# Optimization experiments

Measured on AMD Instinct MI355X. Metric: run time of the kernel, lower is better.

The kernel has to match this reference:

```python
import jax, jax.numpy as jnp
import numpy as np

N_NODES = 50000


def _gcn_conv(x, W, b, src, dst, n):
    # GCNConv (PyG semantics): x' = D^-1/2 (A + I) D^-1/2 (x W) + b
    h = x @ W  # [N, out]
    loop = jnp.arange(n, dtype=src.dtype)
    s = jnp.concatenate([src, loop])  # self-loops appended
    d = jnp.concatenate([dst, loop])
    deg = jax.ops.segment_sum(jnp.ones_like(d, dtype=h.dtype), d, num_segments=n)
    dinv = jnp.where(deg > 0, jax.lax.rsqrt(deg), 0.0)
    norm = dinv[s] * dinv[d]  # [E+N]
    msgs = norm[:, None] * h[s]  # gather: [E+N, out]
    out = jax.ops.segment_sum(msgs, d, num_segments=n)  # scatter-add
    return out + b


def setup_inputs() -> dict:
    key = jax.random.key(0)
    ks = jax.random.split(key, 6)
    n, din, dh, dout, e = N_NODES, 64, 64, 16, 1600000
    x = jax.random.normal(ks[0], (n, din), dtype=jnp.float32)
    edge_index = jax.random.randint(ks[1], (2, e), 0, n, dtype=jnp.int64)
    W1 = jax.random.normal(ks[2], (din, dh), dtype=jnp.float32) / np.sqrt(din)
    b1 = jnp.zeros((dh,), dtype=jnp.float32)
    W2 = jax.random.normal(ks[3], (dh, dout), dtype=jnp.float32) / np.sqrt(dh)
    b2 = jnp.zeros((dout,), dtype=jnp.float32)
    return {"x": x, "edge_index": edge_index, "W1": W1, "b1": b1, "W2": W2, "b2": b2}


def reference(x, edge_index, W1, b1, W2, b2):
    n = x.shape[0]
    src, dst = edge_index[0], edge_index[1]
    h = _gcn_conv(x, W1, b1, src, dst, n)
    h = jax.nn.relu(h)
    h = _gcn_conv(h, W2, b2, src, dst, n)
    return jax.nn.log_softmax(h, axis=1)
```

## Files before the change

### kernel.cpp

```cpp
#include <hip/hip_runtime.h>
#include <hip/hip_bf16.h>
#include <math.h>

#define BSHIFT 6
#define BNODES 64
#define MAXB 1024
#define SORTCAP 4096

__device__ __forceinline__ bool detect_f64(const void* edges, long long nn) {
    const long long* e64 = (const long long*)edges;
    bool ok = true;
#pragma unroll
    for (int i = 0; i < 8; ++i) {
        long long v = e64[i];
        ok = ok && (v >= 0 && v < nn);
    }
    return ok;
}

__device__ __forceinline__ float bf16lo(unsigned int u) {
    return __uint_as_float(u << 16);
}
__device__ __forceinline__ float bf16hi(unsigned int u) {
    return __uint_as_float(u & 0xFFFF0000u);
}
__device__ __forceinline__ float bf16dec(unsigned short u) {
    return __uint_as_float(((unsigned int)u) << 16);
}
__device__ __forceinline__ unsigned short bf16enc(float f) {
    __hip_bfloat16 h = __float2bfloat16(f);
    return *reinterpret_cast<unsigned short*>(&h);
}

__global__ __launch_bounds__(256) void k_hist_gemm1(const void* edges, long long nn,
                                                    long long E, long long epb,
                                                    int nbuckets, int nblk, int* partial,
                                                    const float* __restrict__ x,
                                                    const float* __restrict__ W1,
                                                    unsigned short* __restrict__ h1b) {
    __shared__ __align__(16) char smem[20480];
    int t = threadIdx.x;
    if (blockIdx.x < (unsigned int)nblk) {
        int* cnt = (int*)smem;
        int i = blockIdx.x;
        for (int b = t; b < nbuckets; b += 256) cnt[b] = 0;
        __syncthreads();
        bool f64 = detect_f64(edges, nn);
        long long e0 = (long long)i * epb;
        long long e1 = e0 + epb; if (e1 > E) e1 = E;
        for (long long e = e0 + t; e < e1; e += 256) {
            int d = f64 ? (int)((const long long*)edges)[E + e] : ((const int*)edges)[E + e];
            atomicAdd(&cnt[d >> BSHIFT], 1);
        }
        __syncthreads();
        for (int b = t; b < nbuckets; b += 256) partial[b * nblk + i] = cnt[b];
    } else {
        float (*Ws)[64] = (float(*)[64])smem;
        float (*xs)[64] = (float(*)[64])(smem + 64 * 64 * 4);
        for (int i = t; i < 64 * 64; i += 256) Ws[i >> 6][i & 63] = W1[i];
        long long row0 = (long long)(blockIdx.x - nblk) * 16;
        ((float4*)xs)[t] = ((const float4*)(x + row0 * 64))[t];
        __syncthreads();
        int r = t >> 4, c0 = (t & 15) * 4;
        float4 acc = {0.f, 0.f, 0.f, 0.f};
#pragma unroll
        for (int k = 0; k < 64; ++k) {
            float xv = xs[r][k];
            float4 wv = *((const float4*)&Ws[k][c0]);
            acc.x += xv * wv.x; acc.y += xv * wv.y;
            acc.z += xv * wv.z; acc.w += xv * wv.w;
        }
        ushort4 pk;
        pk.x = bf16enc(acc.x);
        pk.y = bf16enc(acc.y);
        pk.z = bf16enc(acc.z);
        pk.w = bf16enc(acc.w);
        *((ushort4*)(h1b + (row0 + r) * 64 + c0)) = pk;
    }
}

__global__ __launch_bounds__(256) void k_scanB(int* partial, int nblk, int* totals) {
    __shared__ int tmp[256];
    int b = blockIdx.x, t = threadIdx.x;
    int v = (t < nblk) ? partial[b * nblk + t] : 0;
    tmp[t] = v;
    __syncthreads();
    for (int off = 1; off < 256; off <<= 1) {
        int a = (t >= off) ? tmp[t - off] : 0;
        __syncthreads();
        tmp[t] += a;
        __syncthreads();
    }
    if (t < nblk) partial[b * nblk + t] = tmp[t] - v;
    if (t == 255) totals[b] = tmp[255];
}

__global__ __launch_bounds__(1024) void k_scan(const int* __restrict__ totals, int nbuckets,
                                               int* base) {
    __shared__ int tmp[MAXB];
    int t = threadIdx.x;
    int v = (t < nbuckets) ? totals[t] : 0;
    tmp[t] = v;
    __syncthreads();
    for (int off = 1; off < MAXB; off <<= 1) {
        int a = (t >= off) ? tmp[t - off] : 0;
        __syncthreads();
        tmp[t] += a;
        __syncthreads();
    }
    if (t < nbuckets) base[t] = tmp[t] - v;
}

__global__ __launch_bounds__(512) void k_place(const void* edges, long long nn,
                                               long long E, long long epb,
                                               int nbuckets, int nblk,
                                               const int* __restrict__ base,
                                               const int* __restrict__ partial,
                                               unsigned int* keys) {
    __shared__ int cur[MAXB];
    int t = threadIdx.x;
    int i = blockIdx.x;
    for (int b = t; b < nbuckets; b += 512) cur[b] = base[b] + partial[b * nblk + i];
    __syncthreads();
    bool f64 = detect_f64(edges, nn);
    long long e0 = (long long)i * epb;
    long long e1 = e0 + epb; if (e1 > E) e1 = E;
    for (long long e = e0 + t; e < e1; e += 512) {
        int s, d;
        if (f64) {
            const long long* ee = (const long long*)edges;
            s = (int)ee[e]; d = (int)ee[E + e];
        } else {
            const int* ee = (const int*)edges;
            s = ee[e]; d = ee[E + e];
        }
        int pos = atomicAdd(&cur[d >> BSHIFT], 1);
        keys[pos] = (unsigned int)s | ((unsigned int)(d & (BNODES - 1)) << 17);
    }
}

__global__ __launch_bounds__(256) void k_sortdeg(unsigned int* keys,
                                                 const int* __restrict__ base,
                                                 const int* __restrict__ totals,
                                                 int* rowstart, int* counts,
                                                 float* dinv, int n,
                                                 unsigned int* scratch) {
    __shared__ unsigned int kbuf[SORTCAP];
    __shared__ int hist[BNODES];
    __shared__ int cur[BNODES];
    int t = threadIdx.x;
    int bk = blockIdx.x;
    int st = base[bk], c = totals[bk];
    if (t < BNODES) hist[t] = 0;
    __syncthreads();
    bool fits = (c <= SORTCAP);
    if (fits) {
        for (int i = t; i < c; i += 256) {
            unsigned int k = keys[st + i];
            kbuf[i] = k;
            atomicAdd(&hist[k >> 17], 1);
        }
    } else {
        for (int i = t; i < c; i += 256) {
            unsigned int k = keys[st + i];
            scratch[st + i] = k;
            atomicAdd(&hist[k >> 17], 1);
        }
    }
    __syncthreads();
    if (t < 64) {
        int v = hist[t];
        int incl = v;
        for (int o = 1; o < 64; o <<= 1) {
            int other = __shfl_up(incl, o, 64);
            if (t >= o) incl += other;
        }
        int ex = incl - v;
        cur[t] = ex;
        int node = bk * BNODES + t;
        if (node < n) {
            rowstart[node] = st + ex;
            counts[node] = v;
            dinv[node] = rsqrtf((float)v + 1.0f);
        }
    }
    __syncthreads();
    if (fits) {
        for (int i = t; i < c; i += 256) {
            unsigned int k = kbuf[i];
            int pos = atomicAdd(&cur[k >> 17], 1);
            keys[st + pos] = k & 0x1FFFFu;
        }
    } else {
        for (int i = t; i < c; i += 256) {
            unsigned int k = scratch[st + i];
            int pos = atomicAdd(&cur[k >> 17], 1);
            keys[st + pos] = k & 0x1FFFFu;
        }
    }
}

__global__ __launch_bounds__(256) void k_agg64(const int* __restrict__ rowstart,
                                               const int* __restrict__ counts,
                                               const unsigned int* __restrict__ srcs,
                                               const uint2* __restrict__ hb4,
                                               const float* __restrict__ dinv,
                                               const float* __restrict__ b,
                                               const float* __restrict__ W2,
                                               unsigned short* __restrict__ h2b, int n) {
    __shared__ float W2s[64 * 17];
    int t = threadIdx.x;
    for (int i = t; i < 64 * 16; i += 256) W2s[(i >> 4) * 17 + (i & 15)] = W2[i];
    __syncthreads();

    int d = (blockIdx.x * 256 + t) >> 6;
    if (d >= n) return;
    int lane = t & 63;
    unsigned int q = lane >> 4;
    unsigned int fl = lane & 15;
    float di = dinv[d];
    float a0 = 0.f, a1 = 0.f, a2 = 0.f, a3 = 0.f;
    if (q == 0) {
        uint2 u = hb4[(unsigned int)d * 16u + fl];
        a0 = di * bf16lo(u.x); a1 = di * bf16hi(u.x);
        a2 = di * bf16lo(u.y); a3 = di * bf16hi(u.y);
    }
    int start = rowstart[d];
    int cnt = counts[d];
    int k = 0;
    for (; k + 16 <= cnt; k += 16) {
        unsigned int s0 = srcs[start + k + q];
        unsigned int s1 = srcs[start + k + 4 + q];
        unsigned int s2 = srcs[start + k + 8 + q];
        unsigned int s3 = srcs[start + k + 12 + q];
        float dv0 = dinv[s0];
        float dv1 = dinv[s1];
        float dv2 = dinv[s2];
        float dv3 = dinv[s3];
        uint2 u0 = hb4[s0 * 16u + fl];
        uint2 u1 = hb4[s1 * 16u + fl];
        uint2 u2 = hb4[s2 * 16u + fl];
        uint2 u3 = hb4[s3 * 16u + fl];
        a0 = fmaf(dv0, bf16lo(u0.x), a0); a1 = fmaf(dv0, bf16hi(u0.x), a1);
        a2 = fmaf(dv0, bf16lo(u0.y), a2); a3 = fmaf(dv0, bf16hi(u0.y), a3);
        a0 = fmaf(dv1, bf16lo(u1.x), a0); a1 = fmaf(dv1, bf16hi(u1.x), a1);
        a2 = fmaf(dv1, bf16lo(u1.y), a2); a3 = fmaf(dv1, bf16hi(u1.y), a3);
        a0 = fmaf(dv2, bf16lo(u2.x), a0); a1 = fmaf(dv2, bf16hi(u2.x), a1);
        a2 = fmaf(dv2, bf16lo(u2.y), a2); a3 = fmaf(dv2, bf16hi(u2.y), a3);
        a0 = fmaf(dv3, bf16lo(u3.x), a0); a1 = fmaf(dv3, bf16hi(u3.x), a1);
        a2 = fmaf(dv3, bf16lo(u3.y), a2); a3 = fmaf(dv3, bf16hi(u3.y), a3);
    }
    for (; k + 8 <= cnt; k += 8) {
        unsigned int s0 = srcs[start + k + q];
        unsigned int s1 = srcs[start + k + 4 + q];
        float dv0 = dinv[s0];
        float dv1 = dinv[s1];
        uint2 u0 = hb4[s0 * 16u + fl];
        uint2 u1 = hb4[s1 * 16u + fl];
        a0 = fmaf(dv0, bf16lo(u0.x), a0); a1 = fmaf(dv0, bf16hi(u0.x), a1);
        a2 = fmaf(dv0, bf16lo(u0.y), a2); a3 = fmaf(dv0, bf16hi(u0.y), a3);
        a0 = fmaf(dv1, bf16lo(u1.x), a0); a1 = fmaf(dv1, bf16hi(u1.x), a1);
        a2 = fmaf(dv1, bf16lo(u1.y), a2); a3 = fmaf(dv1, bf16hi(u1.y), a3);
    }
    for (; k < cnt; k += 4) {
        int idx = k + (int)q;
        if (idx < cnt) {
            unsigned int s0 = srcs[start + idx];
            float dv0 = dinv[s0];
            uint2 u0 = hb4[s0 * 16u + fl];
            a0 = fmaf(dv0, bf16lo(u0.x), a0); a1 = fmaf(dv0, bf16hi(u0.x), a1);
            a2 = fmaf(dv0, bf16lo(u0.y), a2); a3 = fmaf(dv0, bf16hi(u0.y), a3);
        }
    }
    a0 += __shfl_xor(a0, 16); a0 += __shfl_xor(a0, 32);
    a1 += __shfl_xor(a1, 16); a1 += __shfl_xor(a1, 32);
    a2 += __shfl_xor(a2, 16); a2 += __shfl_xor(a2, 32);
    a3 += __shfl_xor(a3, 16); a3 += __shfl_xor(a3, 32);
    float4 bb = ((const float4*)b)[fl];
    float o0 = fmaxf(di * a0 + bb.x, 0.f);
    float o1 = fmaxf(di * a1 + bb.y, 0.f);
    float o2 = fmaxf(di * a2 + bb.z, 0.f);
    float o3 = fmaxf(di * a3 + bb.w, 0.f);

    int c = lane & 15;
    float acc = 0.f;
#pragma unroll
    for (int j = 0; j < 16; ++j) {
        int kk = (int)q * 16 + j;
        int srcl = (int)q * 20 + (j >> 2);
        float fv;
        if ((j & 3) == 0)      fv = __shfl(o0, srcl);
        else if ((j & 3) == 1) fv = __shfl(o1, srcl);
        else if ((j & 3) == 2) fv = __shfl(o2, srcl);
        else                   fv = __shfl(o3, srcl);
        acc += fv * W2s[kk * 17 + c];
    }
    acc += __shfl_xor(acc, 16);
    acc += __shfl_xor(acc, 32);
    if (lane < 16) h2b[(unsigned int)d * 16u + c] = bf16enc(di * acc);
}

__global__ __launch_bounds__(256) void k_agg16(const int* __restrict__ rowstart,
                                               const int* __restrict__ counts,
                                               const unsigned int* __restrict__ srcs,
                                               const unsigned short* __restrict__ hb,
                                               const float* __restrict__ dinv,
                                               const float* __restrict__ b,
                                               float* __restrict__ out, int n) {
    int g = (blockIdx.x * 256 + threadIdx.x) >> 4;
    if (g >= n) return;
    unsigned int f = threadIdx.x & 15;
    float acc = bf16dec(hb[(unsigned int)g * 16u + f]);
    int start = rowstart[g];
    int cnt = counts[g];
    int k = 0;
    for (; k + 8 <= cnt; k += 8) {
        unsigned int s0 = srcs[start + k];
        unsigned int s1 = srcs[start + k + 1];
        unsigned int s2 = srcs[start + k + 2];
        unsigned int s3 = srcs[start + k + 3];
        unsigned int s4 = srcs[start + k + 4];
        unsigned int s5 = srcs[start + k + 5];
        unsigned int s6 = srcs[start + k + 6];
        unsigned int s7 = srcs[start + k + 7];
        unsigned short u0 = hb[s0 * 16u + f];
        unsigned short u1 = hb[s1 * 16u + f];
        unsigned short u2 = hb[s2 * 16u + f];
        unsigned short u3 = hb[s3 * 16u + f];
        unsigned short u4 = hb[s4 * 16u + f];
        unsigned short u5 = hb[s5 * 16u + f];
        unsigned short u6 = hb[s6 * 16u + f];
        unsigned short u7 = hb[s7 * 16u + f];
        acc += bf16dec(u0); acc += bf16dec(u1); acc += bf16dec(u2); acc += bf16dec(u3);
        acc += bf16dec(u4); acc += bf16dec(u5); acc += bf16dec(u6); acc += bf16dec(u7);
    }
    for (; k < cnt; ++k) acc += bf16dec(hb[srcs[start + k] * 16u + f]);
    float v = dinv[g] * acc + b[f];
    float m = v;
#pragma unroll
    for (int o = 8; o >= 1; o >>= 1) m = fmaxf(m, __shfl_xor(m, o, 16));
    float ex = __expf(v - m);
#pragma unroll
    for (int o = 8; o >= 1; o >>= 1) ex += __shfl_xor(ex, o, 16);
    out[(unsigned int)g * 16u + f] = (v - m) - __logf(ex);
}

extern "C" void kernel_launch(void* const* d_in, const int* in_sizes, int n_in,
                              void* d_out, int out_size, void* d_ws, size_t ws_size,
                              hipStream_t stream) {
    const float* x  = (const float*)d_in[0];
    const void*  ei = d_in[1];
    const float* W1 = (const float*)d_in[2];
    const float* b1 = (const float*)d_in[3];
    const float* W2 = (const float*)d_in[4];
    const float* b2 = (const float*)d_in[5];

    long long dh  = in_sizes[3];
    long long din = in_sizes[2] / dh;
    long long n   = in_sizes[0] / din;
    long long E   = (long long)in_sizes[1] / 2;
    int nbuckets  = (int)((n + BNODES - 1) >> BSHIFT);

    long long epb = 8192;
    while ((E + epb - 1) / epb > 256) epb <<= 1;
    int nblk = (int)((E + epb - 1) / epb);
    int ngemm = (int)(n / 16);

    char* ws = (char*)d_ws;
    auto alloc = [&](size_t bytes) { void* p = ws; ws += (bytes + 255) & ~255ULL; return p; };
    int*   totals   = (int*)alloc(nbuckets * 4);
    int*   base     = (int*)alloc(nbuckets * 4);
    int*   rowstart = (int*)alloc(n * 4);
    int*   counts   = (int*)alloc(n * 4);
    float* dinv     = (float*)alloc(n * 4);
    int*   partial  = (int*)alloc((size_t)nbuckets * nblk * 4);
    unsigned int* keys = (unsigned int*)alloc(E * 4);
    unsigned short* h1b  = (unsigned short*)alloc(n * 64 * 2);
    unsigned short* h2b  = (unsigned short*)alloc(n * 16 * 2);
    unsigned int* sort_scratch = (unsigned int*)alloc(E * 4);

    float* out = (float*)d_out;

    k_hist_gemm1<<<nblk + ngemm, 256, 0, stream>>>(ei, n, E, epb, nbuckets, nblk,
                                                   partial, x, W1, h1b);
    k_scanB<<<nbuckets, 256, 0, stream>>>(partial, nblk, totals);
    k_scan<<<1, 1024, 0, stream>>>(totals, nbuckets, base);
    k_place<<<nblk, 512, 0, stream>>>(ei, n, E, epb, nbuckets, nblk, base, partial, keys);
    k_sortdeg<<<nbuckets, 256, 0, stream>>>(keys, base, totals, rowstart, counts,
                                            dinv, (int)n, sort_scratch);

    k_agg64<<<(int)((n * 64 + 255) / 256), 256, 0, stream>>>(
        rowstart, counts, keys, (const uint2*)h1b, dinv, b1, W2, h2b, (int)n);

    k_agg16<<<(int)((n * 16 + 255) / 256), 256, 0, stream>>>(
        rowstart, counts, keys, h2b, dinv, b2, out, (int)n);
}
```

Before: 110.6 us.

## Fold the bucket-total scan into k_place and k_sortdeg, dropping the k_scan launch

Removes the single-block k_scan kernel. Each k_place block now recomputes the exclusive scan of bucket totals itself, with 256 threads covering four buckets each. Each k_sortdeg block finds its start offset by summing the totals of all earlier buckets with a shared-memory tree reduction. This saves one kernel launch and its serialization point. In exchange, the scan work is repeated in every block, and k_place drops from 512 to 256 threads per block.

Result: slower. 113.0 us (+2.2%).

```diff
diff --git a/kernel.cpp b/kernel.cpp
--- a/kernel.cpp
+++ b/kernel.cpp
@@ -95,37 +95,40 @@
     if (t == 255) totals[b] = tmp[255];
 }
 
-__global__ __launch_bounds__(1024) void k_scan(const int* __restrict__ totals, int nbuckets,
-                                               int* base) {
-    __shared__ int tmp[MAXB];
-    int t = threadIdx.x;
-    int v = (t < nbuckets) ? totals[t] : 0;
-    tmp[t] = v;
-    __syncthreads();
-    for (int off = 1; off < MAXB; off <<= 1) {
-        int a = (t >= off) ? tmp[t - off] : 0;
-        __syncthreads();
-        tmp[t] += a;
-        __syncthreads();
-    }
-    if (t < nbuckets) base[t] = tmp[t] - v;
-}
-
-__global__ __launch_bounds__(512) void k_place(const void* edges, long long nn,
+__global__ __launch_bounds__(256) void k_place(const void* edges, long long nn,
                                                long long E, long long epb,
                                                int nbuckets, int nblk,
-                                               const int* __restrict__ base,
+                                               const int* __restrict__ totals,
                                                const int* __restrict__ partial,
                                                unsigned int* keys) {
     __shared__ int cur[MAXB];
+    __shared__ int tmp[256];
     int t = threadIdx.x;
     int i = blockIdx.x;
-    for (int b = t; b < nbuckets; b += 512) cur[b] = base[b] + partial[b * nblk + i];
+    int i0 = t * 4;
+    int x0 = (i0 + 0 < nbuckets) ? totals[i0 + 0] : 0;
+    int x1 = (i0 + 1 < nbuckets) ? totals[i0 + 1] : 0;
+    int x2 = (i0 + 2 < nbuckets) ? totals[i0 + 2] : 0;
+    int x3 = (i0 + 3 < nbuckets) ? totals[i0 + 3] : 0;
+    int s4 = x0 + x1 + x2 + x3;
+    tmp[t] = s4;
+    __syncthreads();
+    for (int off = 1; off < 256; off <<= 1) {
+        int a = (t >= off) ? tmp[t - off] : 0;
+        __syncthreads();
+        tmp[t] += a;
+        __syncthreads();
+    }
+    int ex = tmp[t] - s4;
+    if (i0 + 0 < nbuckets) cur[i0 + 0] = ex + partial[(i0 + 0) * nblk + i];
+    if (i0 + 1 < nbuckets) cur[i0 + 1] = ex + x0 + partial[(i0 + 1) * nblk + i];
+    if (i0 + 2 < nbuckets) cur[i0 + 2] = ex + x0 + x1 + partial[(i0 + 2) * nblk + i];
+    if (i0 + 3 < nbuckets) cur[i0 + 3] = ex + x0 + x1 + x2 + partial[(i0 + 3) * nblk + i];
     __syncthreads();
     bool f64 = detect_f64(edges, nn);
     long long e0 = (long long)i * epb;
     long long e1 = e0 + epb; if (e1 > E) e1 = E;
-    for (long long e = e0 + t; e < e1; e += 512) {
+    for (long long e = e0 + t; e < e1; e += 256) {
         int s, d;
         if (f64) {
             const long long* ee = (const long long*)edges;
@@ -140,7 +143,6 @@
 }
 
 __global__ __launch_bounds__(256) void k_sortdeg(unsigned int* keys,
-                                                 const int* __restrict__ base,
                                                  const int* __restrict__ totals,
                                                  int* rowstart, int* counts,
                                                  float* dinv, int n,
@@ -148,11 +150,20 @@
     __shared__ unsigned int kbuf[SORTCAP];
     __shared__ int hist[BNODES];
     __shared__ int cur[BNODES];
+    __shared__ int rtmp[256];
     int t = threadIdx.x;
     int bk = blockIdx.x;
-    int st = base[bk], c = totals[bk];
+    int psum = 0;
+    for (int b = t; b < bk; b += 256) psum += totals[b];
+    rtmp[t] = psum;
     if (t < BNODES) hist[t] = 0;
     __syncthreads();
+    for (int off = 128; off > 0; off >>= 1) {
+        if (t < off) rtmp[t] += rtmp[t + off];
+        __syncthreads();
+    }
+    int st = rtmp[0];
+    int c = totals[bk];
     bool fits = (c <= SORTCAP);
     if (fits) {
         for (int i = t; i < c; i += 256) {
@@ -369,7 +380,6 @@
     char* ws = (char*)d_ws;
     auto alloc = [&](size_t bytes) { void* p = ws; ws += (bytes + 255) & ~255ULL; return p; };
     int*   totals   = (int*)alloc(nbuckets * 4);
-    int*   base     = (int*)alloc(nbuckets * 4);
     int*   rowstart = (int*)alloc(n * 4);
     int*   counts   = (int*)alloc(n * 4);
     float* dinv     = (float*)alloc(n * 4);
@@ -384,9 +394,8 @@
     k_hist_gemm1<<<nblk + ngemm, 256, 0, stream>>>(ei, n, E, epb, nbuckets, nblk,
                                                    partial, x, W1, h1b);
     k_scanB<<<nbuckets, 256, 0, stream>>>(partial, nblk, totals);
-    k_scan<<<1, 1024, 0, stream>>>(totals, nbuckets, base);
-    k_place<<<nblk, 512, 0, stream>>>(ei, n, E, epb, nbuckets, nblk, base, partial, keys);
-    k_sortdeg<<<nbuckets, 256, 0, stream>>>(keys, base, totals, rowstart, counts,
+    k_place<<<nblk, 256, 0, stream>>>(ei, n, E, epb, nbuckets, nblk, totals, partial, keys);
+    k_sortdeg<<<nbuckets, 256, 0, stream>>>(keys, totals, rowstart, counts,
                                             dinv, (int)n, sort_scratch);
 
     k_agg64<<<(int)((n * 64 + 255) / 256), 256, 0, stream>>>(
```

## Split layer-1 aggregation into two feature-half passes for cache locality

Applied to the files above, without the earlier changes.

Stores the layer-1 bf16 features as two separate 32-column tables and runs the gather-aggregate twice, once per half. Each table is 3.2MB instead of 6.4MB, so the random neighbour gathers are meant to hit in L2/LLC more often. The first pass writes its post-ReLU half to a temporary buffer, and the second pass reads it back to do the W2 projection. In exchange, the edge list, dinv lookups and kernel launches are doubled, and each gather now fetches 4 bytes per lane instead of 8.

Result: slower. 132.6 us (+19.9%).

```diff
diff --git a/kernel.cpp b/kernel.cpp
--- a/kernel.cpp
+++ b/kernel.cpp
@@ -37,7 +37,8 @@
                                                     int nbuckets, int nblk, int* partial,
                                                     const float* __restrict__ x,
                                                     const float* __restrict__ W1,
-                                                    unsigned short* __restrict__ h1b) {
+                                                    unsigned short* __restrict__ h1lo,
+                                                    unsigned short* __restrict__ h1hi) {
     __shared__ __align__(16) char smem[20480];
     int t = threadIdx.x;
     if (blockIdx.x < (unsigned int)nblk) {
@@ -75,7 +76,9 @@
         pk.y = bf16enc(acc.y);
         pk.z = bf16enc(acc.z);
         pk.w = bf16enc(acc.w);
-        *((ushort4*)(h1b + (row0 + r) * 64 + c0)) = pk;
+        unsigned short* dst = (c0 < 32) ? (h1lo + (row0 + r) * 32 + c0)
+                                        : (h1hi + (row0 + r) * 32 + (c0 - 32));
+        *((ushort4*)dst) = pk;
     }
 }
 
@@ -200,30 +203,23 @@
     }
 }
 
-__global__ __launch_bounds__(256) void k_agg64(const int* __restrict__ rowstart,
-                                               const int* __restrict__ counts,
-                                               const unsigned int* __restrict__ srcs,
-                                               const uint2* __restrict__ hb4,
-                                               const float* __restrict__ dinv,
-                                               const float* __restrict__ b,
-                                               const float* __restrict__ W2,
-                                               unsigned short* __restrict__ h2b, int n) {
-    __shared__ float W2s[64 * 17];
-    int t = threadIdx.x;
-    for (int i = t; i < 64 * 16; i += 256) W2s[(i >> 4) * 17 + (i & 15)] = W2[i];
-    __syncthreads();
-
-    int d = (blockIdx.x * 256 + t) >> 6;
+__global__ __launch_bounds__(256) void k_agg64A(const int* __restrict__ rowstart,
+                                                const int* __restrict__ counts,
+                                                const unsigned int* __restrict__ srcs,
+                                                const unsigned int* __restrict__ tbl,
+                                                const float* __restrict__ dinv,
+                                                const float* __restrict__ b,
+                                                unsigned int* __restrict__ outA, int n) {
+    int d = (blockIdx.x * 256 + threadIdx.x) >> 6;
     if (d >= n) return;
-    int lane = t & 63;
+    int lane = threadIdx.x & 63;
     unsigned int q = lane >> 4;
     unsigned int fl = lane & 15;
     float di = dinv[d];
-    float a0 = 0.f, a1 = 0.f, a2 = 0.f, a3 = 0.f;
+    float a0 = 0.f, a1 = 0.f;
     if (q == 0) {
-        uint2 u = hb4[(unsigned int)d * 16u + fl];
-        a0 = di * bf16lo(u.x); a1 = di * bf16hi(u.x);
-        a2 = di * bf16lo(u.y); a3 = di * bf16hi(u.y);
+        unsigned int u = tbl[(unsigned int)d * 16u + fl];
+        a0 = di * bf16lo(u); a1 = di * bf16hi(u);
     }
     int start = rowstart[d];
     int cnt = counts[d];
@@ -233,66 +229,124 @@
         unsigned int s1 = srcs[start + k + 4 + q];
         unsigned int s2 = srcs[start + k + 8 + q];
         unsigned int s3 = srcs[start + k + 12 + q];
-        float dv0 = dinv[s0];
-        float dv1 = dinv[s1];
-        float dv2 = dinv[s2];
-        float dv3 = dinv[s3];
-        uint2 u0 = hb4[s0 * 16u + fl];
-        uint2 u1 = hb4[s1 * 16u + fl];
-        uint2 u2 = hb4[s2 * 16u + fl];
-        uint2 u3 = hb4[s3 * 16u + fl];
-        a0 = fmaf(dv0, bf16lo(u0.x), a0); a1 = fmaf(dv0, bf16hi(u0.x), a1);
-        a2 = fmaf(dv0, bf16lo(u0.y), a2); a3 = fmaf(dv0, bf16hi(u0.y), a3);
-        a0 = fmaf(dv1, bf16lo(u1.x), a0); a1 = fmaf(dv1, bf16hi(u1.x), a1);
-        a2 = fmaf(dv1, bf16lo(u1.y), a2); a3 = fmaf(dv1, bf16hi(u1.y), a3);
-        a0 = fmaf(dv2, bf16lo(u2.x), a0); a1 = fmaf(dv2, bf16hi(u2.x), a1);
-        a2 = fmaf(dv2, bf16lo(u2.y), a2); a3 = fmaf(dv2, bf16hi(u2.y), a3);
-        a0 = fmaf(dv3, bf16lo(u3.x), a0); a1 = fmaf(dv3, bf16hi(u3.x), a1);
-        a2 = fmaf(dv3, bf16lo(u3.y), a2); a3 = fmaf(dv3, bf16hi(u3.y), a3);
+        float dv0 = dinv[s0], dv1 = dinv[s1], dv2 = dinv[s2], dv3 = dinv[s3];
+        unsigned int u0 = tbl[s0 * 16u + fl];
+        unsigned int u1 = tbl[s1 * 16u + fl];
+        unsigned int u2 = tbl[s2 * 16u + fl];
+        unsigned int u3 = tbl[s3 * 16u + fl];
+        a0 = fmaf(dv0, bf16lo(u0), a0); a1 = fmaf(dv0, bf16hi(u0), a1);
+        a0 = fmaf(dv1, bf16lo(u1), a0); a1 = fmaf(dv1, bf16hi(u1), a1);
+        a0 = fmaf(dv2, bf16lo(u2), a0); a1 = fmaf(dv2, bf16hi(u2), a1);
+        a0 = fmaf(dv3, bf16lo(u3), a0); a1 = fmaf(dv3, bf16hi(u3), a1);
     }
     for (; k + 8 <= cnt; k += 8) {
         unsigned int s0 = srcs[start + k + q];
         unsigned int s1 = srcs[start + k + 4 + q];
-        float dv0 = dinv[s0];
-        float dv1 = dinv[s1];
-        uint2 u0 = hb4[s0 * 16u + fl];
-        uint2 u1 = hb4[s1 * 16u + fl];
-        a0 = fmaf(dv0, bf16lo(u0.x), a0); a1 = fmaf(dv0, bf16hi(u0.x), a1);
-        a2 = fmaf(dv0, bf16lo(u0.y), a2); a3 = fmaf(dv0, bf16hi(u0.y), a3);
-        a0 = fmaf(dv1, bf16lo(u1.x), a0); a1 = fmaf(dv1, bf16hi(u1.x), a1);
-        a2 = fmaf(dv1, bf16lo(u1.y), a2); a3 = fmaf(dv1, bf16hi(u1.y), a3);
+        float dv0 = dinv[s0], dv1 = dinv[s1];
+        unsigned int u0 = tbl[s0 * 16u + fl];
+        unsigned int u1 = tbl[s1 * 16u + fl];
+        a0 = fmaf(dv0, bf16lo(u0), a0); a1 = fmaf(dv0, bf16hi(u0), a1);
+        a0 = fmaf(dv1, bf16lo(u1), a0); a1 = fmaf(dv1, bf16hi(u1), a1);
     }
     for (; k < cnt; k += 4) {
         int idx = k + (int)q;
         if (idx < cnt) {
             unsigned int s0 = srcs[start + idx];
             float dv0 = dinv[s0];
-            uint2 u0 = hb4[s0 * 16u + fl];
-            a0 = fmaf(dv0, bf16lo(u0.x), a0); a1 = fmaf(dv0, bf16hi(u0.x), a1);
-            a2 = fmaf(dv0, bf16lo(u0.y), a2); a3 = fmaf(dv0, bf16hi(u0.y), a3);
+            unsigned int u0 = tbl[s0 * 16u + fl];
+            a0 = fmaf(dv0, bf16lo(u0), a0); a1 = fmaf(dv0, bf16hi(u0), a1);
         }
     }
     a0 += __shfl_xor(a0, 16); a0 += __shfl_xor(a0, 32);
     a1 += __shfl_xor(a1, 16); a1 += __shfl_xor(a1, 32);
-    a2 += __shfl_xor(a2, 16); a2 += __shfl_xor(a2, 32);
-    a3 += __shfl_xor(a3, 16); a3 += __shfl_xor(a3, 32);
-    float4 bb = ((const float4*)b)[fl];
-    float o0 = fmaxf(di * a0 + bb.x, 0.f);
-    float o1 = fmaxf(di * a1 + bb.y, 0.f);
-    float o2 = fmaxf(di * a2 + bb.z, 0.f);
-    float o3 = fmaxf(di * a3 + bb.w, 0.f);
+    if (q == 0) {
+        float2 bb = ((const float2*)b)[fl];
+        float o0 = fmaxf(di * a0 + bb.x, 0.f);
+        float o1 = fmaxf(di * a1 + bb.y, 0.f);
+        outA[(unsigned int)d * 16u + fl] =
+            (unsigned int)bf16enc(o0) | ((unsigned int)bf16enc(o1) << 16);
+    }
+}
+
+__global__ __launch_bounds__(256) void k_agg64B(const int* __restrict__ rowstart,
+                                                const int* __restrict__ counts,
+                                                const unsigned int* __restrict__ srcs,
+                                                const unsigned int* __restrict__ tbl,
+                                                const float* __restrict__ dinv,
+                                                const float* __restrict__ b,
+                                                const float* __restrict__ W2,
+                                                const unsigned int* __restrict__ outA,
+                                                unsigned short* __restrict__ h2b, int n) {
+    __shared__ float W2s[64 * 17];
+    int t = threadIdx.x;
+    for (int i = t; i < 64 * 16; i += 256) W2s[(i >> 4) * 17 + (i & 15)] = W2[i];
+    __syncthreads();
+
+    int d = (blockIdx.x * 256 + t) >> 6;
+    if (d >= n) return;
+    int lane = t & 63;
+    unsigned int q = lane >> 4;
+    unsigned int fl = lane & 15;
+    float di = dinv[d];
+    float a0 = 0.f, a1 = 0.f;
+    if (q == 0) {
+        unsigned int u = tbl[(unsigned int)d * 16u + fl];
+        a0 = di * bf16lo(u); a1 = di * bf16hi(u);
+    }
+    int start = rowstart[d];
+    int cnt = counts[d];
+    int k = 0;
+    for (; k + 16 <= cnt; k += 16) {
+        unsigned int s0 = srcs[start + k + q];
+        unsigned int s1 = srcs[start + k + 4 + q];
+        unsigned int s2 = srcs[start + k + 8 + q];
+        unsigned int s3 = srcs[start + k + 12 + q];
+        float dv0 = dinv[s0], dv1 = dinv[s1], dv2 = dinv[s2], dv3 = dinv[s3];
+        unsigned int u0 = tbl[s0 * 16u + fl];
+        unsigned int u1 = tbl[s1 * 16u + fl];
+        unsigned int u2 = tbl[s2 * 16u + fl];
+        unsigned int u3 = tbl[s3 * 16u + fl];
+        a0 = fmaf(dv0, bf16lo(u0), a0); a1 = fmaf(dv0, bf16hi(u0), a1);
+        a0 = fmaf(dv1, bf16lo(u1), a0); a1 = fmaf(dv1, bf16hi(u1), a1);
+        a0 = fmaf(dv2, bf16lo(u2), a0); a1 = fmaf(dv2, bf16hi(u2), a1);
+        a0 = fmaf(dv3, bf16lo(u3), a0); a1 = fmaf(dv3, bf16hi(u3), a1);
+    }
+    for (; k + 8 <= cnt; k += 8) {
+        unsigned int s0 = srcs[start + k + q];
+        unsigned int s1 = srcs[start + k + 4 + q];
+        float dv0 = dinv[s0], dv1 = dinv[s1];
+        unsigned int u0 = tbl[s0 * 16u + fl];
+        unsigned int u1 = tbl[s1 * 16u + fl];
+        a0 = fmaf(dv0, bf16lo(u0), a0); a1 = fmaf(dv0, bf16hi(u0), a1);
+        a0 = fmaf(dv1, bf16lo(u1), a0); a1 = fmaf(dv1, bf16hi(u1), a1);
+    }
+    for (; k < cnt; k += 4) {
+        int idx = k + (int)q;
+        if (idx < cnt) {
+            unsigned int s0 = srcs[start + idx];
+            float dv0 = dinv[s0];
+            unsigned int u0 = tbl[s0 * 16u + fl];
+            a0 = fmaf(dv0, bf16lo(u0), a0); a1 = fmaf(dv0, bf16hi(u0), a1);
+        }
+    }
+    a0 += __shfl_xor(a0, 16); a0 += __shfl_xor(a0, 32);
+    a1 += __shfl_xor(a1, 16); a1 += __shfl_xor(a1, 32);
+    float2 bb = ((const float2*)(b + 32))[fl];
+    float o2 = fmaxf(di * a0 + bb.x, 0.f);
+    float o3 = fmaxf(di * a1 + bb.y, 0.f);
+    unsigned int ulo = outA[(unsigned int)d * 16u + fl];
+    float o0 = bf16lo(ulo);
+    float o1 = bf16hi(ulo);
 
     int c = lane & 15;
     float acc = 0.f;
 #pragma unroll
     for (int j = 0; j < 16; ++j) {
         int kk = (int)q * 16 + j;
-        int srcl = (int)q * 20 + (j >> 2);
-        float fv;
-        if ((j & 3) == 0)      fv = __shfl(o0, srcl);
-        else if ((j & 3) == 1) fv = __shfl(o1, srcl);
-        else if ((j & 3) == 2) fv = __shfl(o2, srcl);
-        else                   fv = __shfl(o3, srcl);
+        int srcl = (int)q * 16 + (((unsigned)kk & 31u) >> 1);
+        float fvl = (j & 1) ? o1 : o0;
+        float fvh = (j & 1) ? o3 : o2;
+        float fv = __shfl((q >= 2) ? fvh : fvl, srcl);
         acc += fv * W2s[kk * 17 + c];
     }
     acc += __shfl_xor(acc, 16);
@@ -375,22 +429,26 @@
     float* dinv     = (float*)alloc(n * 4);
     int*   partial  = (int*)alloc((size_t)nbuckets * nblk * 4);
     unsigned int* keys = (unsigned int*)alloc(E * 4);
-    unsigned short* h1b  = (unsigned short*)alloc(n * 64 * 2);
+    unsigned short* h1lo = (unsigned short*)alloc(n * 32 * 2);
+    unsigned short* h1hi = (unsigned short*)alloc(n * 32 * 2);
+    unsigned int*   outA = (unsigned int*)alloc(n * 32 * 2);
     unsigned short* h2b  = (unsigned short*)alloc(n * 16 * 2);
     unsigned int* sort_scratch = (unsigned int*)alloc(E * 4);
 
     float* out = (float*)d_out;
 
     k_hist_gemm1<<<nblk + ngemm, 256, 0, stream>>>(ei, n, E, epb, nbuckets, nblk,
-                                                   partial, x, W1, h1b);
+                                                   partial, x, W1, h1lo, h1hi);
     k_scanB<<<nbuckets, 256, 0, stream>>>(partial, nblk, totals);
     k_scan<<<1, 1024, 0, stream>>>(totals, nbuckets, base);
     k_place<<<nblk, 512, 0, stream>>>(ei, n, E, epb, nbuckets, nblk, base, partial, keys);
     k_sortdeg<<<nbuckets, 256, 0, stream>>>(keys, base, totals, rowstart, counts,
                                             dinv, (int)n, sort_scratch);
 
-    k_agg64<<<(int)((n * 64 + 255) / 256), 256, 0, stream>>>(
-        rowstart, counts, keys, (const uint2*)h1b, dinv, b1, W2, h2b, (int)n);
+    k_agg64A<<<(int)((n * 64 + 255) / 256), 256, 0, stream>>>(
+        rowstart, counts, keys, (const unsigned int*)h1lo, dinv, b1, outA, (int)n);
+    k_agg64B<<<(int)((n * 64 + 255) / 256), 256, 0, stream>>>(
+        rowstart, counts, keys, (const unsigned int*)h1hi, dinv, b1, W2, outA, h2b, (int)n);
 
     k_agg16<<<(int)((n * 16 + 255) / 256), 256, 0, stream>>>(
         rowstart, counts, keys, h2b, dinv, b2, out, (int)n);
```
